# Kernel optimization log

Measured on AMD Instinct MI355X. Metric: run time of the kernel, lower is better.

Reference implementation:

```python
import jax, jax.numpy as jnp
import numpy as np

N_NODES = 50000
N_EDGES = 800000
N_GRAPHS = 128
ORIG_FEA = 92
NBR_FEA = 41
H = 64
N_CONV = 3
BN_EPS = 1e-5


def setup_inputs() -> dict:
    key = jax.random.key(0)
    ks = jax.random.split(key, 16)
    x = jax.random.normal(ks[0], (N_NODES, ORIG_FEA), dtype=jnp.float32)
    edge_attr = jax.random.normal(ks[1], (N_EDGES, NBR_FEA), dtype=jnp.float32)
    edge_index = jax.random.randint(ks[2], (2, N_EDGES), 0, N_NODES)
    batch = jnp.sort(jax.random.randint(ks[3], (N_NODES,), 0, N_GRAPHS))
    s_emb1 = 1.0 / np.sqrt(ORIG_FEA)
    s_emb2 = 1.0 / np.sqrt(NBR_FEA)
    s_conv = 1.0 / np.sqrt(3 * H)
    s_h = 1.0 / np.sqrt(H)
    return {
        "x": x,
        "edge_attr": edge_attr,
        "edge_index": edge_index,
        "batch": batch,
        "W_emb1": jax.random.uniform(ks[4], (ORIG_FEA, H), jnp.float32, -s_emb1, s_emb1),
        "b_emb1": jnp.zeros((H,), jnp.float32),
        "W_emb2": jax.random.uniform(ks[5], (NBR_FEA, H), jnp.float32, -s_emb2, s_emb2),
        "b_emb2": jnp.zeros((H,), jnp.float32),
        "Wf": jax.random.uniform(ks[6], (N_CONV, 3 * H, H), jnp.float32, -s_conv, s_conv),
        "bf": jnp.zeros((N_CONV, H), jnp.float32),
        "Ws": jax.random.uniform(ks[7], (N_CONV, 3 * H, H), jnp.float32, -s_conv, s_conv),
        "bs": jnp.zeros((N_CONV, H), jnp.float32),
        "gamma": jnp.ones((N_CONV, H), jnp.float32),
        "beta": jnp.zeros((N_CONV, H), jnp.float32),
        "W1": jax.random.uniform(ks[8], (H, H), jnp.float32, -s_h, s_h),
        "b1": jnp.zeros((H,), jnp.float32),
        "W2": jax.random.uniform(ks[9], (H, H), jnp.float32, -s_h, s_h),
        "b2": jnp.zeros((H,), jnp.float32),
        "Wo": jax.random.uniform(ks[10], (H, 1), jnp.float32, -s_h, s_h),
        "bo": jnp.zeros((1,), jnp.float32),
    }


def _batch_norm(h, g, b):
    # training-mode BatchNorm1d: biased batch statistics
    mu = jnp.mean(h, axis=0)
    var = jnp.var(h, axis=0)
    return (h - mu) * jax.lax.rsqrt(var + BN_EPS) * g + b


def reference(x, edge_attr, edge_index, batch, W_emb1, b_emb1, W_emb2, b_emb2,
              Wf, bf, Ws, bs, gamma, beta, W1, b1, W2, b2, Wo, bo):
    src = edge_index[0]  # x_j (source)
    dst = edge_index[1]  # x_i (target, aggregation index)
    h = x @ W_emb1 + b_emb1              # [N, H]
    e = edge_attr @ W_emb2 + b_emb2      # [E, H]
    for a in range(N_CONV):
        # CGConv: z_ij = [x_i, x_j, e_ij]; msg = sigmoid(lin_f(z)) * softplus(lin_s(z))
        z = jnp.concatenate([h[dst], h[src], e], axis=1)       # [E, 3H]
        msg = jax.nn.sigmoid(z @ Wf[a] + bf[a]) * jax.nn.softplus(z @ Ws[a] + bs[a])
        h = h + jax.ops.segment_sum(msg, dst, num_segments=N_NODES)
        h = _batch_norm(h, gamma[a], beta[a])
        if a != N_CONV - 1:
            h = jax.nn.relu(h)
        # dropout ratio is 0 -> no-op
    # JK='last' -> node representation is final h; mean pooling per graph
    sums = jax.ops.segment_sum(h, batch, num_segments=N_GRAPHS)              # [G, H]
    cnts = jax.ops.segment_sum(jnp.ones((N_NODES,), h.dtype), batch, num_segments=N_GRAPHS)
    y = sums / jnp.maximum(cnts, 1.0)[:, None]
    y = jax.nn.softplus(y @ W1 + b1)
    y = jax.nn.softplus(y @ W2 + b2)
    y = (y @ Wo + bo).squeeze(-1)  # [G]
    return y
```

## Files before the change

kernel.cpp:

```cpp
#include <hip/hip_runtime.h>
#include <hip/hip_bf16.h>
#include <math.h>

#define N_NODES 50000
#define N_EDGES 800000
#define N_GRAPHS 128
#define ORIG_FEA 92
#define NBR_FEA 41
#define H 64
#define N_CONV 3
#define BN_EPS 1e-5f

__device__ __forceinline__ float sigmoidf_(float x) {
    return __fdividef(1.f, 1.f + __expf(-x));
}
__device__ __forceinline__ float softplusf_(float x) {
    return fmaxf(x, 0.f) + __logf(1.f + __expf(-fabsf(x)));
}

__global__ __launch_bounds__(256) void fold_kernel(
    const float* __restrict__ W_emb2, const float* __restrict__ b_emb2,
    const float* __restrict__ Wf, const float* __restrict__ bf,
    const float* __restrict__ Ws, const float* __restrict__ bs,
    float* __restrict__ W2f, float* __restrict__ W2s,
    float* __restrict__ cf, float* __restrict__ cs) {
    int a = blockIdx.x >> 1, gate = blockIdx.x & 1;
    const float* W = (gate ? Ws : Wf) + a * 192 * H + 128 * H;
    const float* bias = (gate ? bs : bf) + a * H;
    float* Wout = (gate ? W2s : W2f) + a * NBR_FEA * H;
    float* cout = (gate ? cs : cf) + a * H;
    for (int idx = threadIdx.x; idx < NBR_FEA * H; idx += blockDim.x) {
        int k = idx / H, j = idx % H;
        float acc = 0.f;
        for (int m = 0; m < H; ++m) acc += W_emb2[k * H + m] * W[m * H + j];
        Wout[idx] = acc;
    }
    for (int j = threadIdx.x; j < H; j += blockDim.x) {
        float acc = bias[j];
        for (int m = 0; m < H; ++m) acc += b_emb2[m] * W[m * H + j];
        cout[j] = acc;
    }
}

__global__ __launch_bounds__(256) void embed_kernel(
    const float* __restrict__ x, const float* __restrict__ W,
    const float* __restrict__ b, float* __restrict__ h) {
    __shared__ float lw[ORIG_FEA * H];
    for (int i = threadIdx.x; i < ORIG_FEA * H; i += blockDim.x) lw[i] = W[i];
    __syncthreads();
    int lane = threadIdx.x & 63;
    int wid = (blockIdx.x * blockDim.x + threadIdx.x) >> 6;
    int nw = (gridDim.x * blockDim.x) >> 6;
    for (int n = wid; n < N_NODES; n += nw) {
        int nu = __builtin_amdgcn_readfirstlane(n);
        const float* xr = x + (size_t)nu * ORIG_FEA;
        float acc = b[lane];
#pragma unroll
        for (int k = 0; k < ORIG_FEA; ++k) acc += xr[k] * lw[k * H + lane];
        h[(size_t)nu * H + lane] = acc;
    }
}

__global__ __launch_bounds__(256) void node_proj_kernel(
    const float* __restrict__ h,
    const float* __restrict__ Wf, const float* __restrict__ Ws,
    float* __restrict__ Pf, float* __restrict__ Qf,
    float* __restrict__ Ps, float* __restrict__ Qs,
    float* __restrict__ hsum) {
    __shared__ float lw[4 * H * H];
    for (int i = threadIdx.x; i < H * H; i += blockDim.x) {
        lw[i] = Wf[i];
        lw[H * H + i] = Wf[H * H + i];
        lw[2 * H * H + i] = Ws[i];
        lw[3 * H * H + i] = Ws[H * H + i];
    }
    __syncthreads();
    int lane = threadIdx.x & 63;
    int wid = (blockIdx.x * blockDim.x + threadIdx.x) >> 6;
    int nw = (gridDim.x * blockDim.x) >> 6;
    for (int n = wid; n < N_NODES; n += nw) {
        int nu = __builtin_amdgcn_readfirstlane(n);
        const float* hr = h + (size_t)nu * H;
        float pf = 0.f, qf = 0.f, ps = 0.f, qs = 0.f;
#pragma unroll
        for (int k = 0; k < H; ++k) {
            float s = hr[k];
            pf += s * lw[k * H + lane];
            qf += s * lw[H * H + k * H + lane];
            ps += s * lw[2 * H * H + k * H + lane];
            qs += s * lw[3 * H * H + k * H + lane];
        }
        size_t o = (size_t)nu * H + lane;
        Pf[o] = pf; Qf[o] = qf; Ps[o] = ps; Qs[o] = qs;
        hsum[o] = hr[lane];
    }
}

__global__ __launch_bounds__(256) void edge_kernel(
    const int* __restrict__ ei, const float* __restrict__ ea,
    const float* __restrict__ Pf, const float* __restrict__ Qf,
    const float* __restrict__ Ps, const float* __restrict__ Qs,
    const float* __restrict__ W2f, const float* __restrict__ W2s,
    const float* __restrict__ cf, const float* __restrict__ cs,
    float* __restrict__ hsum) {
    int lane = threadIdx.x & 63;
    float wf[NBR_FEA], ws2[NBR_FEA];
#pragma unroll
    for (int k = 0; k < NBR_FEA; ++k) {
        wf[k] = W2f[k * H + lane];
        ws2[k] = W2s[k * H + lane];
    }
    float cfl = cf[lane], csl = cs[lane];
    int wid = (blockIdx.x * blockDim.x + threadIdx.x) >> 6;
    int nw = (gridDim.x * blockDim.x) >> 6;
    for (int e = wid; e < N_EDGES; e += nw) {
        int eu = __builtin_amdgcn_readfirstlane(e);
        int src = ei[eu];
        int dst = ei[N_EDGES + eu];
        float af = cfl + Pf[(size_t)dst * H + lane] + Qf[(size_t)src * H + lane];
        float as = csl + Ps[(size_t)dst * H + lane] + Qs[(size_t)src * H + lane];
        const float* er = ea + (size_t)eu * NBR_FEA;
#pragma unroll
        for (int k = 0; k < NBR_FEA; ++k) {
            float s = er[k];
            af += s * wf[k];
            as += s * ws2[k];
        }
        atomicAdd(&hsum[(size_t)dst * H + lane], sigmoidf_(af) * softplusf_(as));
    }
}

__global__ __launch_bounds__(256) void bn_stats_kernel(
    const float* __restrict__ hsum, float* __restrict__ stats) {
    int lane = threadIdx.x & 63;
    int wl = threadIdx.x >> 6;
    int wid = (blockIdx.x * blockDim.x + threadIdx.x) >> 6;
    int nw = (gridDim.x * blockDim.x) >> 6;
    float s = 0.f, s2 = 0.f;
    for (int n = wid; n < N_NODES; n += nw) {
        float v = hsum[(size_t)n * H + lane];
        s += v;
        s2 += v * v;
    }
    __shared__ float ls[4 * 2 * H];
    ls[wl * 2 * H + lane] = s;
    ls[wl * 2 * H + H + lane] = s2;
    __syncthreads();
    if (wl == 0) {
        float a = ls[lane] + ls[2 * H + lane] + ls[4 * H + lane] + ls[6 * H + lane];
        float b = ls[H + lane] + ls[3 * H + lane] + ls[5 * H + lane] + ls[7 * H + lane];
        atomicAdd(&stats[lane], a);
        atomicAdd(&stats[H + lane], b);
    }
}

__global__ __launch_bounds__(256) void bn_apply_kernel(
    const float* __restrict__ hsum, const float* __restrict__ stats,
    const float* __restrict__ gamma, const float* __restrict__ beta,
    float* __restrict__ h, int relu) {
    int idx0 = blockIdx.x * blockDim.x + threadIdx.x;
    int stride = gridDim.x * blockDim.x;
    const float inv_n = 1.f / (float)N_NODES;
    for (int idx = idx0; idx < N_NODES * H; idx += stride) {
        int j = idx & (H - 1);
        float mu = stats[j] * inv_n;
        float var = stats[H + j] * inv_n - mu * mu;
        float inv = rsqrtf(var + BN_EPS);
        float v = (hsum[idx] - mu) * inv * gamma[j] + beta[j];
        if (relu) v = fmaxf(v, 0.f);
        h[idx] = v;
    }
}

__global__ __launch_bounds__(256) void pool_kernel(
    const float* __restrict__ h, const int* __restrict__ batch,
    float* __restrict__ gsum, float* __restrict__ gcnt) {
    int lane = threadIdx.x & 63;
    int wid = (blockIdx.x * blockDim.x + threadIdx.x) >> 6;
    int nw = (gridDim.x * blockDim.x) >> 6;
    for (int n = wid; n < N_NODES; n += nw) {
        int nu = __builtin_amdgcn_readfirstlane(n);
        int g = batch[nu];
        atomicAdd(&gsum[(size_t)g * H + lane], h[(size_t)nu * H + lane]);
        if (lane == 0) atomicAdd(&gcnt[g], 1.f);
    }
}

__global__ __launch_bounds__(64) void mlp_kernel(
    const float* __restrict__ gsum, const float* __restrict__ gcnt,
    const float* __restrict__ W1, const float* __restrict__ b1,
    const float* __restrict__ W2, const float* __restrict__ b2,
    const float* __restrict__ Wo, const float* __restrict__ bo,
    float* __restrict__ out) {
    int g = blockIdx.x;
    int lane = threadIdx.x;
    __shared__ float y[H];
    float cnt = fmaxf(gcnt[g], 1.f);
    y[lane] = gsum[(size_t)g * H + lane] / cnt;
    __syncthreads();
    float acc = b1[lane];
#pragma unroll
    for (int k = 0; k < H; ++k) acc += y[k] * W1[k * H + lane];
    float y1 = softplusf_(acc);
    __syncthreads();
    y[lane] = y1;
    __syncthreads();
    acc = b2[lane];
#pragma unroll
    for (int k = 0; k < H; ++k) acc += y[k] * W2[k * H + lane];
    float y2 = softplusf_(acc);
    float t = y2 * Wo[lane];
#pragma unroll
    for (int o = 32; o > 0; o >>= 1) t += __shfl_down(t, o, 64);
    if (lane == 0) out[g] = t + bo[0];
}

extern "C" void kernel_launch(void* const* d_in, const int* in_sizes, int n_in,
                              void* d_out, int out_size, void* d_ws, size_t ws_size,
                              hipStream_t stream) {
    const float* x = (const float*)d_in[0];
    const float* ea = (const float*)d_in[1];
    const int* ei = (const int*)d_in[2];
    const int* batch = (const int*)d_in[3];
    const float* W_emb1 = (const float*)d_in[4];
    const float* b_emb1 = (const float*)d_in[5];
    const float* W_emb2 = (const float*)d_in[6];
    const float* b_emb2 = (const float*)d_in[7];
    const float* Wf = (const float*)d_in[8];
    const float* bf = (const float*)d_in[9];
    const float* Ws = (const float*)d_in[10];
    const float* bs = (const float*)d_in[11];
    const float* gamma = (const float*)d_in[12];
    const float* beta = (const float*)d_in[13];
    const float* W1 = (const float*)d_in[14];
    const float* b1 = (const float*)d_in[15];
    const float* W2 = (const float*)d_in[16];
    const float* b2 = (const float*)d_in[17];
    const float* Wo = (const float*)d_in[18];
    const float* bo = (const float*)d_in[19];
    float* out = (float*)d_out;

    float* w = (float*)d_ws;
    float* stats = w;
    float* gsum = w + 3 * 2 * H;
    float* gcnt = gsum + N_GRAPHS * H;
    float* h = gcnt + N_GRAPHS;
    float* hsum = h + (size_t)N_NODES * H;
    float* Pf = hsum + (size_t)N_NODES * H;
    float* Qf = Pf + (size_t)N_NODES * H;
    float* Ps = Qf + (size_t)N_NODES * H;
    float* Qs = Ps + (size_t)N_NODES * H;
    float* W2f = Qs + (size_t)N_NODES * H;
    float* W2s = W2f + 3 * NBR_FEA * H;
    float* cf = W2s + 3 * NBR_FEA * H;
    float* cs = cf + 3 * H;

    hipMemsetAsync(w, 0, (3 * 2 * H + N_GRAPHS * H + N_GRAPHS) * sizeof(float), stream);

    fold_kernel<<<6, 256, 0, stream>>>(W_emb2, b_emb2, Wf, bf, Ws, bs, W2f, W2s, cf, cs);
    embed_kernel<<<512, 256, 0, stream>>>(x, W_emb1, b_emb1, h);

    for (int a = 0; a < N_CONV; ++a) {
        node_proj_kernel<<<512, 256, 0, stream>>>(h, Wf + a * 192 * H, Ws + a * 192 * H,
                                                  Pf, Qf, Ps, Qs, hsum);
        edge_kernel<<<1024, 256, 0, stream>>>(ei, ea, Pf, Qf, Ps, Qs,
                                              W2f + a * NBR_FEA * H, W2s + a * NBR_FEA * H,
                                              cf + a * H, cs + a * H, hsum);
        bn_stats_kernel<<<256, 256, 0, stream>>>(hsum, stats + a * 2 * H);
        bn_apply_kernel<<<2048, 256, 0, stream>>>(hsum, stats + a * 2 * H,
                                                  gamma + a * H, beta + a * H, h,
                                                  a != N_CONV - 1 ? 1 : 0);
    }

    pool_kernel<<<784, 256, 0, stream>>>(h, batch, gsum, gcnt);
    mlp_kernel<<<128, 64, 0, stream>>>(gsum, gcnt, W1, b1, W2, b2, Wo, bo, out);
}
```

Measured before the change: 1.291 ms.

## Interleave gate/filter projections as float2 and use packed FMA in edge kernel

Node projections and folded edge weights are stored interleaved (filter, core) per channel, so each edge gathers one 8-byte value per lane per endpoint instead of two separate 4-byte values. The edge dot product uses 2-wide vector FMAs that can map to packed fp32 math. The edge grid is doubled and launch bounds ask for two blocks per CU. An empty asm barrier keeps the weights in registers. This targets gather transactions and VALU count in the dominant edge kernel, at the cost of register pressure from the 41-entry float2 weight array.

```diff
diff --git a/kernel.cpp b/kernel.cpp
--- a/kernel.cpp
+++ b/kernel.cpp
@@ -11,6 +11,8 @@
 #define N_CONV 3
 #define BN_EPS 1e-5f
 
+typedef float v2f __attribute__((ext_vector_type(2)));
+
 __device__ __forceinline__ float sigmoidf_(float x) {
     return __fdividef(1.f, 1.f + __expf(-x));
 }
@@ -22,23 +24,22 @@
     const float* __restrict__ W_emb2, const float* __restrict__ b_emb2,
     const float* __restrict__ Wf, const float* __restrict__ bf,
     const float* __restrict__ Ws, const float* __restrict__ bs,
-    float* __restrict__ W2f, float* __restrict__ W2s,
-    float* __restrict__ cf, float* __restrict__ cs) {
+    float* __restrict__ W2c, float* __restrict__ cfs) {
     int a = blockIdx.x >> 1, gate = blockIdx.x & 1;
     const float* W = (gate ? Ws : Wf) + a * 192 * H + 128 * H;
     const float* bias = (gate ? bs : bf) + a * H;
-    float* Wout = (gate ? W2s : W2f) + a * NBR_FEA * H;
-    float* cout = (gate ? cs : cf) + a * H;
+    float* Wout = W2c + a * NBR_FEA * 2 * H;
+    float* cout = cfs + a * 2 * H;
     for (int idx = threadIdx.x; idx < NBR_FEA * H; idx += blockDim.x) {
         int k = idx / H, j = idx % H;
         float acc = 0.f;
         for (int m = 0; m < H; ++m) acc += W_emb2[k * H + m] * W[m * H + j];
-        Wout[idx] = acc;
+        Wout[k * 2 * H + 2 * j + gate] = acc;
     }
     for (int j = threadIdx.x; j < H; j += blockDim.x) {
         float acc = bias[j];
         for (int m = 0; m < H; ++m) acc += b_emb2[m] * W[m * H + j];
-        cout[j] = acc;
+        cout[2 * j + gate] = acc;
     }
 }
 
@@ -64,8 +65,7 @@
 __global__ __launch_bounds__(256) void node_proj_kernel(
     const float* __restrict__ h,
     const float* __restrict__ Wf, const float* __restrict__ Ws,
-    float* __restrict__ Pf, float* __restrict__ Qf,
-    float* __restrict__ Ps, float* __restrict__ Qs,
+    float* __restrict__ NPi, float* __restrict__ NPj,
     float* __restrict__ hsum) {
     __shared__ float lw[4 * H * H];
     for (int i = threadIdx.x; i < H * H; i += blockDim.x) {
@@ -90,43 +90,41 @@
             ps += s * lw[2 * H * H + k * H + lane];
             qs += s * lw[3 * H * H + k * H + lane];
         }
-        size_t o = (size_t)nu * H + lane;
-        Pf[o] = pf; Qf[o] = qf; Ps[o] = ps; Qs[o] = qs;
-        hsum[o] = hr[lane];
-    }
-}
-
-__global__ __launch_bounds__(256) void edge_kernel(
+        v2f pi; pi.x = pf; pi.y = ps;
+        v2f pj; pj.x = qf; pj.y = qs;
+        *(v2f*)&NPi[(size_t)nu * 2 * H + 2 * lane] = pi;
+        *(v2f*)&NPj[(size_t)nu * 2 * H + 2 * lane] = pj;
+        hsum[(size_t)nu * H + lane] = hr[lane];
+    }
+}
+
+__global__ __launch_bounds__(256, 2) void edge_kernel(
     const int* __restrict__ ei, const float* __restrict__ ea,
-    const float* __restrict__ Pf, const float* __restrict__ Qf,
-    const float* __restrict__ Ps, const float* __restrict__ Qs,
-    const float* __restrict__ W2f, const float* __restrict__ W2s,
-    const float* __restrict__ cf, const float* __restrict__ cs,
+    const float* __restrict__ NPi, const float* __restrict__ NPj,
+    const float* __restrict__ W2c, const float* __restrict__ cfs,
     float* __restrict__ hsum) {
     int lane = threadIdx.x & 63;
-    float wf[NBR_FEA], ws2[NBR_FEA];
-#pragma unroll
-    for (int k = 0; k < NBR_FEA; ++k) {
-        wf[k] = W2f[k * H + lane];
-        ws2[k] = W2s[k * H + lane];
-    }
-    float cfl = cf[lane], csl = cs[lane];
+    v2f w[NBR_FEA];
+#pragma unroll
+    for (int k = 0; k < NBR_FEA; ++k)
+        w[k] = *(const v2f*)&W2c[k * 2 * H + 2 * lane];
+    v2f c2 = *(const v2f*)&cfs[2 * lane];
+#pragma unroll
+    for (int k = 0; k < NBR_FEA; ++k) asm volatile("" : "+v"(w[k]));
     int wid = (blockIdx.x * blockDim.x + threadIdx.x) >> 6;
     int nw = (gridDim.x * blockDim.x) >> 6;
     for (int e = wid; e < N_EDGES; e += nw) {
         int eu = __builtin_amdgcn_readfirstlane(e);
         int src = ei[eu];
         int dst = ei[N_EDGES + eu];
-        float af = cfl + Pf[(size_t)dst * H + lane] + Qf[(size_t)src * H + lane];
-        float as = csl + Ps[(size_t)dst * H + lane] + Qs[(size_t)src * H + lane];
+        v2f pi = *(const v2f*)&NPi[(size_t)dst * 2 * H + 2 * lane];
+        v2f pj = *(const v2f*)&NPj[(size_t)src * 2 * H + 2 * lane];
+        v2f acc = c2 + pi + pj;
         const float* er = ea + (size_t)eu * NBR_FEA;
 #pragma unroll
-        for (int k = 0; k < NBR_FEA; ++k) {
-            float s = er[k];
-            af += s * wf[k];
-            as += s * ws2[k];
-        }
-        atomicAdd(&hsum[(size_t)dst * H + lane], sigmoidf_(af) * softplusf_(as));
+        for (int k = 0; k < NBR_FEA; ++k) acc += w[k] * er[k];
+        float msg = sigmoidf_(acc.x) * softplusf_(acc.y);
+        atomicAdd(&hsum[(size_t)dst * H + lane], msg);
     }
 }
 
@@ -246,26 +244,22 @@
     float* gcnt = gsum + N_GRAPHS * H;
     float* h = gcnt + N_GRAPHS;
     float* hsum = h + (size_t)N_NODES * H;
-    float* Pf = hsum + (size_t)N_NODES * H;
-    float* Qf = Pf + (size_t)N_NODES * H;
-    float* Ps = Qf + (size_t)N_NODES * H;
-    float* Qs = Ps + (size_t)N_NODES * H;
-    float* W2f = Qs + (size_t)N_NODES * H;
-    float* W2s = W2f + 3 * NBR_FEA * H;
-    float* cf = W2s + 3 * NBR_FEA * H;
-    float* cs = cf + 3 * H;
+    float* NPi = hsum + (size_t)N_NODES * H;
+    float* NPj = NPi + (size_t)N_NODES * 2 * H;
+    float* W2c = NPj + (size_t)N_NODES * 2 * H;
+    float* cfs = W2c + 3 * NBR_FEA * 2 * H;
 
     hipMemsetAsync(w, 0, (3 * 2 * H + N_GRAPHS * H + N_GRAPHS) * sizeof(float), stream);
 
-    fold_kernel<<<6, 256, 0, stream>>>(W_emb2, b_emb2, Wf, bf, Ws, bs, W2f, W2s, cf, cs);
+    fold_kernel<<<6, 256, 0, stream>>>(W_emb2, b_emb2, Wf, bf, Ws, bs, W2c, cfs);
     embed_kernel<<<512, 256, 0, stream>>>(x, W_emb1, b_emb1, h);
 
     for (int a = 0; a < N_CONV; ++a) {
         node_proj_kernel<<<512, 256, 0, stream>>>(h, Wf + a * 192 * H, Ws + a * 192 * H,
-                                                  Pf, Qf, Ps, Qs, hsum);
-        edge_kernel<<<1024, 256, 0, stream>>>(ei, ea, Pf, Qf, Ps, Qs,
-                                              W2f + a * NBR_FEA * H, W2s + a * NBR_FEA * H,
-                                              cf + a * H, cs + a * H, hsum);
+                                                  NPi, NPj, hsum);
+        edge_kernel<<<2048, 256, 0, stream>>>(ei, ea, NPi, NPj,
+                                              W2c + a * NBR_FEA * 2 * H,
+                                              cfs + a * 2 * H, hsum);
         bn_stats_kernel<<<256, 256, 0, stream>>>(hsum, stats + a * 2 * H);
         bn_apply_kernel<<<2048, 256, 0, stream>>>(hsum, stats + a * 2 * H,
                                                   gamma + a * H, beta + a * H, h,
```

After: 1.233 ms. -4.5%, faster.
